# Optimization experiments

Hardware: AMD Instinct MI355X
Metric: run time of the kernel (lower is better)

The kernel has to match this reference:

```python
import jax, jax.numpy as jnp
import numpy as np

B, T, C, H = 4, 2048, 1024, 16


def setup_inputs() -> dict:
    key = jax.random.key(0)
    k1, k2, k3 = jax.random.split(key, 3)
    x = jax.random.normal(k1, (B, T, C), dtype=jnp.float32)
    W_qkv = jax.random.normal(k2, (C, 3 * C), dtype=jnp.float32) * 0.02
    W_proj = jax.random.normal(k3, (C, C), dtype=jnp.float32) * 0.02
    return {"x": x, "W_qkv": W_qkv, "W_proj": W_proj}


def reference(x, W_qkv, W_proj):
    Bc, Tc, Cc = x.shape
    D = Cc // H
    qkv = x @ W_qkv                          # [B,T,3C]
    k, q, v = jnp.split(qkv, 3, axis=-1)     # split order k,q,v as in source
    q = q.reshape(Bc, Tc, H, D)
    k = k.reshape(Bc, Tc, H, D)
    v = v.reshape(Bc, Tc, H, D)
    # NOTE: module scales by full C**-0.5, not head_dim**-0.5
    scale = jnp.asarray(Cc, x.dtype) ** -0.5
    wei = jnp.einsum("bqhd,bkhd->bhqk", q, k) * scale      # [B,H,T,T]
    causal = jnp.tril(jnp.ones((Tc, Tc), dtype=bool))
    wei = jnp.where(causal[None, None], wei, jnp.asarray(-jnp.inf, x.dtype))
    att = jax.nn.softmax(wei, axis=-1)
    out = jnp.einsum("bhqk,bkhd->bqhd", att, v).reshape(Bc, Tc, Cc)
    return out @ W_proj
```

## Files before the change

### kernel.cpp

```cpp
#include <hip/hip_runtime.h>
#include <hip/hip_bf16.h>

#define B_   4
#define T_   2048
#define C_   1024
#define H_   16
#define D_   64
#define NQKV 3072
#define M_   (B_*T_)

typedef __attribute__((ext_vector_type(8))) short bf16x8;
typedef __attribute__((ext_vector_type(4))) short bf16x4;
typedef __attribute__((ext_vector_type(4))) float f32x4;
typedef __hip_bfloat16 bf16;

__device__ inline short f2bs(float f) {
    bf16 h = __float2bfloat16(f);
    return *(short*)&h;
}

__device__ inline float exp2g(float f) { return __builtin_amdgcn_exp2f(f); }

__device__ inline void async_ld16(const bf16* g, const short* l) {
    __builtin_amdgcn_global_load_lds(
        (const __attribute__((address_space(1))) void*)g,
        (__attribute__((address_space(3))) void*)l, 16, 0, 0);
}

__global__ __launch_bounds__(256) void prep(const float* __restrict__ x,
                                            const float* __restrict__ Wqkv,
                                            const float* __restrict__ Wproj,
                                            bf16* __restrict__ xb,
                                            bf16* __restrict__ wqkv_t,
                                            bf16* __restrict__ wproj_t) {
    __shared__ short t[32][33];
    const int bid = blockIdx.x;
    if (bid < 4096) {
        const long i = ((long)bid * 256 + threadIdx.x) * 8;
        const float4 a = *(const float4*)(x + i);
        const float4 bq = *(const float4*)(x + i + 4);
        bf16x8 o;
        o[0] = f2bs(a.x); o[1] = f2bs(a.y); o[2] = f2bs(a.z); o[3] = f2bs(a.w);
        o[4] = f2bs(bq.x); o[5] = f2bs(bq.y); o[6] = f2bs(bq.z); o[7] = f2bs(bq.w);
        *(bf16x8*)(xb + i) = o;
        return;
    }
    const float* in;  bf16* out;  int R, Ccol, r0, c0;
    if (bid < 7168) {
        const int b2 = bid - 4096;
        in = Wqkv; out = wqkv_t; R = C_; Ccol = NQKV;
        c0 = (b2 % 96) * 32; r0 = (b2 / 96) * 32;
    } else {
        const int b3 = bid - 7168;
        in = Wproj; out = wproj_t; R = C_; Ccol = C_;
        c0 = (b3 % 32) * 32; r0 = (b3 / 32) * 32;
    }
    const int xx = threadIdx.x & 31, yy = threadIdx.x >> 5;
#pragma unroll
    for (int i = 0; i < 4; i++)
        t[yy + 8*i][xx] = f2bs(in[(long)(r0 + yy + 8*i) * Ccol + c0 + xx]);
    __syncthreads();
#pragma unroll
    for (int i = 0; i < 4; i++)
        ((short*)out)[(long)(c0 + yy + 8*i) * R + r0 + xx] = t[xx][yy + 8*i];
}

template<int MODE>
__global__ __launch_bounds__(256) void gemm_bt(const bf16* __restrict__ A,
                                               const bf16* __restrict__ Bt,
                                               float* __restrict__ outp,
                                               bf16* __restrict__ qb,
                                               bf16* __restrict__ kb,
                                               bf16* __restrict__ vbT,
                                               int K, int N) {
    __shared__ __align__(16) short SMEM[18432];
    short* As = SMEM;
    short* Bs = SMEM + 8192;
    const int tid  = threadIdx.x;
    const int w    = tid >> 6, lane = tid & 63;
    const int g    = lane >> 4, ln = lane & 15;
    const int m0   = blockIdx.y * 128, n0 = blockIdx.x * 128;
    const int wm   = w & 1, wn = w >> 1;

    f32x4 acc[4][4] = {};

    for (int k0 = 0; k0 < K; k0 += 64) {
#pragma unroll
        for (int i = 0; i < 4; i++) {
            const int s   = w * 256 + i * 64 + lane;
            const int row = s >> 3, c8 = (s & 7) ^ ((s >> 3) & 7);
            async_ld16(A  + (long)(m0 + row) * K + k0 + c8 * 8, &As[s * 8]);
            async_ld16(Bt + (long)(n0 + row) * K + k0 + c8 * 8, &Bs[s * 8]);
        }
        __syncthreads();

#pragma unroll
        for (int kh = 0; kh < 2; kh++) {
            bf16x8 af[4], bfr[4];
#pragma unroll
            for (int i = 0; i < 4; i++)
                af[i]  = *(const bf16x8*)&As[(wm * 64 + i * 16 + ln) * 64 + ((kh * 4 + g) ^ (ln & 7)) * 8];
#pragma unroll
            for (int j = 0; j < 4; j++)
                bfr[j] = *(const bf16x8*)&Bs[(wn * 64 + j * 16 + ln) * 64 + ((kh * 4 + g) ^ (ln & 7)) * 8];
#pragma unroll
            for (int i = 0; i < 4; i++)
#pragma unroll
                for (int j = 0; j < 4; j++)
                    acc[i][j] = __builtin_amdgcn_mfma_f32_16x16x32_bf16(af[i], bfr[j], acc[i][j], 0, 0, 0);
        }
        __syncthreads();
    }

    if (MODE == 0 && n0 >= 2048) {
        short* Vt = SMEM;
#pragma unroll
        for (int i = 0; i < 4; i++)
#pragma unroll
            for (int j = 0; j < 4; j++)
#pragma unroll
                for (int r = 0; r < 4; r++) {
                    const int tl = wm * 64 + i * 16 + g * 4 + r;
                    const int dl = wn * 64 + j * 16 + ln;
                    Vt[dl * 144 + tl] = f2bs(acc[i][j][r]);
                }
        __syncthreads();
        const int b  = m0 >> 11, tb = m0 & (T_ - 1);
        const int h0 = (n0 - 2048) >> 6;
#pragma unroll
        for (int ii = 0; ii < 8; ii++) {
            const int s = ii * 256 + tid;
            const int dl = s >> 4, t16 = s & 15;
            const bf16x8 v = *(const bf16x8*)&Vt[dl * 144 + t16 * 8];
            const int h = h0 + (dl >> 6), d = dl & 63;
            *(bf16x8*)&vbT[(((long)(b * H_ + h)) * D_ + d) * T_ + tb + t16 * 8] = v;
        }
        return;
    }

#pragma unroll
    for (int i = 0; i < 4; i++) {
#pragma unroll
        for (int j = 0; j < 4; j++) {
#pragma unroll
            for (int r = 0; r < 4; r++) {
                const int row = m0 + wm * 64 + i * 16 + g * 4 + r;
                const int col = n0 + wn * 64 + j * 16 + ln;
                if (MODE == 1) {
                    outp[(long)row * N + col] = acc[i][j][r];
                } else {
                    const int b = row >> 11, t = row & (T_ - 1);
                    const int seg = col >> 10;
                    const int c = col & (C_ - 1), h = c >> 6, d = c & 63;
                    if (seg == 0)
                        kb[(((long)(b * H_ + h)) * T_ + t) * D_ + d] = __float2bfloat16(acc[i][j][r]);
                    else
                        qb[(((long)(b * H_ + h)) * T_ + t) * D_ + d] =
                            __float2bfloat16(acc[i][j][r] * (0.03125f * 1.44269504f));
                }
            }
        }
    }
}


__device__ inline void subtile(const bf16x8& qf0, const bf16x8& qf1,
                               f32x4* o, f32x4& l,
                               const short* Ks, const short* Vs, short* myP,
                               int q0, int kbase, int h2, int w, int g, int ln,
                               const bf16x8& ones) {
    f32x4 s[4] = {};
    __builtin_amdgcn_s_setprio(1);
#pragma unroll
    for (int kj = 0; kj < 4; kj++) {
        const int krow = h2 * 64 + kj * 16 + ln;
        const bf16x8 kf0 = *(const bf16x8*)&Ks[krow * 64 + ((0 + g) ^ (krow & 7)) * 8];
        s[kj] = __builtin_amdgcn_mfma_f32_16x16x32_bf16(qf0, kf0, s[kj], 0, 0, 0);
        const bf16x8 kf1 = *(const bf16x8*)&Ks[krow * 64 + ((4 + g) ^ (krow & 7)) * 8];
        s[kj] = __builtin_amdgcn_mfma_f32_16x16x32_bf16(qf1, kf1, s[kj], 0, 0, 0);
    }
    __builtin_amdgcn_s_setprio(0);
    const int rowg = q0 + w * 16 + g * 4;
    if (kbase == q0) {
#pragma unroll
        for (int kj = 0; kj < 4; kj++) {
            const int key = kbase + kj * 16 + ln;
#pragma unroll
            for (int r = 0; r < 4; r++) {
                float p = exp2g(s[kj][r]);
                p = (key <= rowg + r) ? p : 0.f;
                const int prow = g * 4 + r;
                const int pc8 = (kj * 2 + (ln >> 3)) ^ (prow & 7);
                myP[prow * 64 + pc8 * 8 + (ln & 7)] = f2bs(p);
            }
        }
    } else {
#pragma unroll
        for (int kj = 0; kj < 4; kj++) {
#pragma unroll
            for (int r = 0; r < 4; r++) {
                const int prow = g * 4 + r;
                const int pc8 = (kj * 2 + (ln >> 3)) ^ (prow & 7);
                myP[prow * 64 + pc8 * 8 + (ln & 7)] = f2bs(exp2g(s[kj][r]));
            }
        }
    }
    asm volatile("s_waitcnt lgkmcnt(0)" ::: "memory");
    const bf16x8 pf0 = *(const bf16x8*)&myP[ln * 64 + ((0 + g) ^ (ln & 7)) * 8];
    const bf16x8 pf1 = *(const bf16x8*)&myP[ln * 64 + ((4 + g) ^ (ln & 7)) * 8];
    l = __builtin_amdgcn_mfma_f32_16x16x32_bf16(ones, pf0, l, 0, 0, 0);
    l = __builtin_amdgcn_mfma_f32_16x16x32_bf16(ones, pf1, l, 0, 0, 0);
    __builtin_amdgcn_s_setprio(1);
#pragma unroll
    for (int nb = 0; nb < 4; nb++) {
        const int drow = nb * 16 + ln;
        const bf16x8 vf0 = *(const bf16x8*)&Vs[drow * 128 + ((h2 * 8 + 0 + g) ^ (drow & 7)) * 8];
        o[nb] = __builtin_amdgcn_mfma_f32_16x16x32_bf16(vf0, pf0, o[nb], 0, 0, 0);
        const bf16x8 vf1 = *(const bf16x8*)&Vs[drow * 128 + ((h2 * 8 + 4 + g) ^ (drow & 7)) * 8];
        o[nb] = __builtin_amdgcn_mfma_f32_16x16x32_bf16(vf1, pf1, o[nb], 0, 0, 0);
    }
    __builtin_amdgcn_s_setprio(0);
}

__device__ inline void subtile_ab(const bf16x8& qfA0, const bf16x8& qfA1,
                                  const bf16x8& qfB0, const bf16x8& qfB1,
                                  f32x4* oA, f32x4& lA, f32x4* oB, f32x4& lB,
                                  const short* Ks, const short* Vs, short* myP,
                                  int q0A, int kbase, int h2, int w, int g, int ln,
                                  const bf16x8& ones, bool diagA) {
    f32x4 sA[4] = {}, sB[4] = {};
    __builtin_amdgcn_s_setprio(1);
#pragma unroll
    for (int kj = 0; kj < 4; kj++) {
        const int krow = h2 * 64 + kj * 16 + ln;
        const bf16x8 kf0 = *(const bf16x8*)&Ks[krow * 64 + ((0 + g) ^ (krow & 7)) * 8];
        const bf16x8 kf1 = *(const bf16x8*)&Ks[krow * 64 + ((4 + g) ^ (krow & 7)) * 8];
        sA[kj] = __builtin_amdgcn_mfma_f32_16x16x32_bf16(qfA0, kf0, sA[kj], 0, 0, 0);
        sA[kj] = __builtin_amdgcn_mfma_f32_16x16x32_bf16(qfA1, kf1, sA[kj], 0, 0, 0);
        sB[kj] = __builtin_amdgcn_mfma_f32_16x16x32_bf16(qfB0, kf0, sB[kj], 0, 0, 0);
        sB[kj] = __builtin_amdgcn_mfma_f32_16x16x32_bf16(qfB1, kf1, sB[kj], 0, 0, 0);
    }
    __builtin_amdgcn_s_setprio(0);
    const int rowg = q0A + w * 16 + g * 4;
    if (diagA) {
#pragma unroll
        for (int kj = 0; kj < 4; kj++) {
            const int key = kbase + kj * 16 + ln;
#pragma unroll
            for (int r = 0; r < 4; r++) {
                float p = exp2g(sA[kj][r]);
                p = (key <= rowg + r) ? p : 0.f;
                const int prow = g * 4 + r;
                const int pc8 = (kj * 2 + (ln >> 3)) ^ (prow & 7);
                myP[prow * 64 + pc8 * 8 + (ln & 7)] = f2bs(p);
            }
        }
    } else {
#pragma unroll
        for (int kj = 0; kj < 4; kj++)
#pragma unroll
            for (int r = 0; r < 4; r++) {
                const int prow = g * 4 + r;
                const int pc8 = (kj * 2 + (ln >> 3)) ^ (prow & 7);
                myP[prow * 64 + pc8 * 8 + (ln & 7)] = f2bs(exp2g(sA[kj][r]));
            }
    }
    asm volatile("s_waitcnt lgkmcnt(0)" ::: "memory");
    const bf16x8 pfA0 = *(const bf16x8*)&myP[ln * 64 + ((0 + g) ^ (ln & 7)) * 8];
    const bf16x8 pfA1 = *(const bf16x8*)&myP[ln * 64 + ((4 + g) ^ (ln & 7)) * 8];
    lA = __builtin_amdgcn_mfma_f32_16x16x32_bf16(ones, pfA0, lA, 0, 0, 0);
    lA = __builtin_amdgcn_mfma_f32_16x16x32_bf16(ones, pfA1, lA, 0, 0, 0);
#pragma unroll
    for (int kj = 0; kj < 4; kj++)
#pragma unroll
        for (int r = 0; r < 4; r++) {
            const int prow = g * 4 + r;
            const int pc8 = (kj * 2 + (ln >> 3)) ^ (prow & 7);
            myP[prow * 64 + pc8 * 8 + (ln & 7)] = f2bs(exp2g(sB[kj][r]));
        }
    __builtin_amdgcn_s_setprio(1);
#pragma unroll
    for (int nb = 0; nb < 4; nb++) {
        const int drow = nb * 16 + ln;
        const bf16x8 vf0 = *(const bf16x8*)&Vs[drow * 128 + ((h2 * 8 + 0 + g) ^ (drow & 7)) * 8];
        oA[nb] = __builtin_amdgcn_mfma_f32_16x16x32_bf16(vf0, pfA0, oA[nb], 0, 0, 0);
        const bf16x8 vf1 = *(const bf16x8*)&Vs[drow * 128 + ((h2 * 8 + 4 + g) ^ (drow & 7)) * 8];
        oA[nb] = __builtin_amdgcn_mfma_f32_16x16x32_bf16(vf1, pfA1, oA[nb], 0, 0, 0);
    }
    __builtin_amdgcn_s_setprio(0);
    asm volatile("s_waitcnt lgkmcnt(0)" ::: "memory");
    const bf16x8 pfB0 = *(const bf16x8*)&myP[ln * 64 + ((0 + g) ^ (ln & 7)) * 8];
    const bf16x8 pfB1 = *(const bf16x8*)&myP[ln * 64 + ((4 + g) ^ (ln & 7)) * 8];
    lB = __builtin_amdgcn_mfma_f32_16x16x32_bf16(ones, pfB0, lB, 0, 0, 0);
    lB = __builtin_amdgcn_mfma_f32_16x16x32_bf16(ones, pfB1, lB, 0, 0, 0);
    __builtin_amdgcn_s_setprio(1);
#pragma unroll
    for (int nb = 0; nb < 4; nb++) {
        const int drow = nb * 16 + ln;
        const bf16x8 vf0 = *(const bf16x8*)&Vs[drow * 128 + ((h2 * 8 + 0 + g) ^ (drow & 7)) * 8];
        oB[nb] = __builtin_amdgcn_mfma_f32_16x16x32_bf16(vf0, pfB0, oB[nb], 0, 0, 0);
        const bf16x8 vf1 = *(const bf16x8*)&Vs[drow * 128 + ((h2 * 8 + 4 + g) ^ (drow & 7)) * 8];
        oB[nb] = __builtin_amdgcn_mfma_f32_16x16x32_bf16(vf1, pfB1, oB[nb], 0, 0, 0);
    }
    __builtin_amdgcn_s_setprio(0);
}

__global__ __launch_bounds__(256, 2) void flash(const bf16* __restrict__ qb,
                                                const bf16* __restrict__ kb,
                                                const bf16* __restrict__ vbT,
                                                bf16* __restrict__ att) {
    __shared__ __align__(16) short Ks[128 * 64];
    __shared__ __align__(16) short Vs[64 * 128];
    __shared__ __align__(16) short Ps[4 * 16 * 64];
    const int tid = threadIdx.x, w = tid >> 6, lane = tid & 63;
    const int g = lane >> 4, ln = lane & 15;
    const int lin = blockIdx.x;
    const int bh = lin & 63, j = lin >> 6;
    const int b = bh >> 4, h = bh & 15;
    const int q0A = j * 64, q0B = (15 - j) * 64;
    const int q0C = (16 + j) * 64, q0D = (31 - j) * 64;

    const bf16* qpA = qb + ((long)bh * T_ + q0A + w * 16 + ln) * D_;
    const bf16* qpB = qb + ((long)bh * T_ + q0B + w * 16 + ln) * D_;
    const bf16* qpC = qb + ((long)bh * T_ + q0C + w * 16 + ln) * D_;
    const bf16* qpD = qb + ((long)bh * T_ + q0D + w * 16 + ln) * D_;
    const bf16x8 qfA0 = *(const bf16x8*)(qpA + g * 8);
    const bf16x8 qfA1 = *(const bf16x8*)(qpA + 32 + g * 8);
    const bf16x8 qfB0 = *(const bf16x8*)(qpB + g * 8);
    const bf16x8 qfB1 = *(const bf16x8*)(qpB + 32 + g * 8);
    const bf16x8 qfC0 = *(const bf16x8*)(qpC + g * 8);
    const bf16x8 qfC1 = *(const bf16x8*)(qpC + 32 + g * 8);
    const bf16x8 qfD0 = *(const bf16x8*)(qpD + g * 8);
    const bf16x8 qfD1 = *(const bf16x8*)(qpD + 32 + g * 8);

    bf16x8 ones;
#pragma unroll
    for (int i = 0; i < 8; i++) ones[i] = 0x3F80;

    f32x4 oA[4] = {}, oB[4] = {}, oC[4] = {}, oD[4] = {};
    f32x4 lA = {}, lB = {}, lC = {}, lD = {};
    short* myP = &Ps[w * 16 * 64];

    const int nst = (q0D + 64 + 127) >> 7;
    for (int s = 0; s < nst; s++) {
        const int k0 = s * 128;
        bf16x8 kr[4], vr[4];
#pragma unroll
        for (int i = 0; i < 4; i++) {
            const int cc = i * 256 + tid;
            kr[i] = *(const bf16x8*)&kb [((long)bh * T_ + k0 + (cc >> 3)) * D_ + (cc & 7) * 8];
            vr[i] = *(const bf16x8*)&vbT[((long)bh * D_ + (cc >> 4)) * T_ + k0 + (cc & 15) * 8];
        }
        __syncthreads();
#pragma unroll
        for (int i = 0; i < 4; i++) {
            const int cc = i * 256 + tid;
            const int key = cc >> 3, c8 = cc & 7;
            *(bf16x8*)&Ks[key * 64 + (c8 ^ (key & 7)) * 8] = kr[i];
            const int d = cc >> 4, c16 = cc & 15;
            *(bf16x8*)&Vs[d * 128 + (c16 ^ (d & 7)) * 8] = vr[i];
        }
        __syncthreads();

#pragma unroll
        for (int h2 = 0; h2 < 2; h2++) {
            const int kbase = k0 + h2 * 64;
            if (kbase <= q0A + 63)
                subtile_ab(qfA0, qfA1, qfB0, qfB1, oA, lA, oB, lB,
                           Ks, Vs, myP, q0A, kbase, h2, w, g, ln, ones,
                           kbase == q0A);
            else if (kbase <= q0B + 63)
                subtile(qfB0, qfB1, oB, lB, Ks, Vs, myP, q0B, kbase, h2, w, g, ln, ones);
            if (kbase <= q0C + 63)
                subtile_ab(qfC0, qfC1, qfD0, qfD1, oC, lC, oD, lD,
                           Ks, Vs, myP, q0C, kbase, h2, w, g, ln, ones,
                           kbase == q0C);
            else if (kbase <= q0D + 63)
                subtile(qfD0, qfD1, oD, lD, Ks, Vs, myP, q0D, kbase, h2, w, g, ln, ones);
        }
    }

#pragma unroll
    for (int ti = 0; ti < 4; ti++) {
        const f32x4* o = (ti == 0) ? oA : (ti == 1) ? oB : (ti == 2) ? oC : oD;
        const float lv = (ti == 0) ? lA[0] : (ti == 1) ? lB[0] : (ti == 2) ? lC[0] : lD[0];
        const int q0 = (ti == 0) ? q0A : (ti == 1) ? q0B : (ti == 2) ? q0C : q0D;
        const float invl = 1.f / lv;
        const int q = q0 + w * 16 + ln;
#pragma unroll
        for (int nb = 0; nb < 4; nb++) {
            bf16x4 pk;
#pragma unroll
            for (int r = 0; r < 4; r++) pk[r] = f2bs(o[nb][r] * invl);
            *(bf16x4*)&att[((long)b * T_ + q) * C_ + h * D_ + nb * 16 + g * 4] = pk;
        }
    }
}

extern "C" void kernel_launch(void* const* d_in, const int* in_sizes, int n_in,
                              void* d_out, int out_size, void* d_ws, size_t ws_size,
                              hipStream_t stream) {
    const float* x     = (const float*)d_in[0];
    const float* Wqkv  = (const float*)d_in[1];
    const float* Wproj = (const float*)d_in[2];
    float* out = (float*)d_out;

    char* ws = (char*)d_ws;
    bf16* wqkv_t  = (bf16*)(ws);
    bf16* wproj_t = (bf16*)(ws + 6291456);
    bf16* qb      = (bf16*)(ws + 8388608);
    bf16* kb      = (bf16*)(ws + 25165824);
    bf16* vbT     = (bf16*)(ws + 41943040);
    bf16* xb      = (bf16*)(ws + 58720256);
    bf16* att     = xb;
    (void)ws_size; (void)in_sizes; (void)n_in; (void)out_size;

    prep<<<dim3(8192), dim3(256), 0, stream>>>(x, Wqkv, Wproj, xb, wqkv_t, wproj_t);
    gemm_bt<0><<<dim3(NQKV / 128, M_ / 128), dim3(256), 0, stream>>>(
        xb, wqkv_t, (float*)nullptr, qb, kb, vbT, C_, NQKV);
    flash<<<dim3(512), dim3(256), 0, stream>>>(qb, kb, vbT, att);
    gemm_bt<1><<<dim3(C_ / 128, M_ / 128), dim3(256), 0, stream>>>(
        att, wproj_t, out, (bf16*)nullptr, (bf16*)nullptr, (bf16*)nullptr, C_, C_);
}
```

Before: 247.3 us.

## Double-buffer K/V tiles in LDS with async global-to-LDS loads

Staging of K and V tiles now uses async global_load_lds directly into shared memory instead of going through registers. The XOR swizzle moves to the global source address so the LDS layout stays the same. Two LDS buffers let the next tile's load be issued before computing on the current one, with one barrier per iteration instead of two. This aims to hide global load latency and cut register pressure. The cost is double the K/V LDS footprint, which reduces headroom for two blocks per CU, and correctness depends on the barrier waiting for the outstanding async loads.

```diff
diff --git a/kernel.cpp b/kernel.cpp
--- a/kernel.cpp
+++ b/kernel.cpp
@@ -305,12 +305,24 @@
     __builtin_amdgcn_s_setprio(0);
 }
 
+__device__ inline void stage_kv(const bf16* kbase_p, const bf16* vbase_p,
+                                short* KsB, short* VsB, int k0, int tid) {
+#pragma unroll
+    for (int i = 0; i < 4; i++) {
+        const int cc = i * 256 + tid;
+        const int key = cc >> 3, kc8 = (cc & 7) ^ (key & 7);
+        async_ld16(kbase_p + (long)(k0 + key) * D_ + kc8 * 8, &KsB[cc * 8]);
+        const int d = cc >> 4, vc16 = (cc & 15) ^ (d & 7);
+        async_ld16(vbase_p + (long)d * T_ + k0 + vc16 * 8, &VsB[cc * 8]);
+    }
+}
+
 __global__ __launch_bounds__(256, 2) void flash(const bf16* __restrict__ qb,
                                                 const bf16* __restrict__ kb,
                                                 const bf16* __restrict__ vbT,
                                                 bf16* __restrict__ att) {
-    __shared__ __align__(16) short Ks[128 * 64];
-    __shared__ __align__(16) short Vs[64 * 128];
+    __shared__ __align__(16) short Ks[2][128 * 64];
+    __shared__ __align__(16) short Vs[2][64 * 128];
     __shared__ __align__(16) short Ps[4 * 16 * 64];
     const int tid = threadIdx.x, w = tid >> 6, lane = tid & 63;
     const int g = lane >> 4, ln = lane & 15;
@@ -341,43 +353,35 @@
     f32x4 lA = {}, lB = {}, lC = {}, lD = {};
     short* myP = &Ps[w * 16 * 64];
 
+    const bf16* kbase_p = kb  + (long)bh * T_ * D_;
+    const bf16* vbase_p = vbT + (long)bh * D_ * T_;
+
     const int nst = (q0D + 64 + 127) >> 7;
+    stage_kv(kbase_p, vbase_p, Ks[0], Vs[0], 0, tid);
+    __syncthreads();
     for (int s = 0; s < nst; s++) {
         const int k0 = s * 128;
-        bf16x8 kr[4], vr[4];
-#pragma unroll
-        for (int i = 0; i < 4; i++) {
-            const int cc = i * 256 + tid;
-            kr[i] = *(const bf16x8*)&kb [((long)bh * T_ + k0 + (cc >> 3)) * D_ + (cc & 7) * 8];
-            vr[i] = *(const bf16x8*)&vbT[((long)bh * D_ + (cc >> 4)) * T_ + k0 + (cc & 15) * 8];
-        }
-        __syncthreads();
-#pragma unroll
-        for (int i = 0; i < 4; i++) {
-            const int cc = i * 256 + tid;
-            const int key = cc >> 3, c8 = cc & 7;
-            *(bf16x8*)&Ks[key * 64 + (c8 ^ (key & 7)) * 8] = kr[i];
-            const int d = cc >> 4, c16 = cc & 15;
-            *(bf16x8*)&Vs[d * 128 + (c16 ^ (d & 7)) * 8] = vr[i];
-        }
-        __syncthreads();
+        const int cur = s & 1;
+        if (s + 1 < nst)
+            stage_kv(kbase_p, vbase_p, Ks[cur ^ 1], Vs[cur ^ 1], k0 + 128, tid);
 
 #pragma unroll
         for (int h2 = 0; h2 < 2; h2++) {
             const int kbase = k0 + h2 * 64;
             if (kbase <= q0A + 63)
                 subtile_ab(qfA0, qfA1, qfB0, qfB1, oA, lA, oB, lB,
-                           Ks, Vs, myP, q0A, kbase, h2, w, g, ln, ones,
+                           Ks[cur], Vs[cur], myP, q0A, kbase, h2, w, g, ln, ones,
                            kbase == q0A);
             else if (kbase <= q0B + 63)
-                subtile(qfB0, qfB1, oB, lB, Ks, Vs, myP, q0B, kbase, h2, w, g, ln, ones);
+                subtile(qfB0, qfB1, oB, lB, Ks[cur], Vs[cur], myP, q0B, kbase, h2, w, g, ln, ones);
             if (kbase <= q0C + 63)
                 subtile_ab(qfC0, qfC1, qfD0, qfD1, oC, lC, oD, lD,
-                           Ks, Vs, myP, q0C, kbase, h2, w, g, ln, ones,
+                           Ks[cur], Vs[cur], myP, q0C, kbase, h2, w, g, ln, ones,
                            kbase == q0C);
             else if (kbase <= q0D + 63)
-                subtile(qfD0, qfD1, oD, lD, Ks, Vs, myP, q0D, kbase, h2, w, g, ln, ones);
-        }
+                subtile(qfD0, qfD1, oD, lD, Ks[cur], Vs[cur], myP, q0D, kbase, h2, w, g, ln, ones);
+        }
+        __syncthreads();
     }
 
 #pragma unroll
```

Measured after the change: 238.3 us, median of 2. -3.6%, faster.
